# Optimization experiments

Hardware: AMD Instinct MI355X
Metric: run time of the kernel (lower is better)

Reference implementation:

```python
import jax, jax.numpy as jnp
import numpy as np

B, M, R = 2, 2048, 256
H, DH = 16, 64
ROPE_THETA = 10000.0


def setup_inputs() -> dict:
    key = jax.random.key(0)
    ks = jax.random.split(key, 9)
    d = H * DH
    inp = {
        "Pq": jax.random.normal(ks[0], (B, M, R), jnp.float32),
        "Pk": jax.random.normal(ks[1], (B, M, R), jnp.float32),
        "Pv": jax.random.normal(ks[2], (B, M, R), jnp.float32),
        "Vq": jax.random.normal(ks[3], (R, d), jnp.float32) / np.sqrt(R),
        "Vk": jax.random.normal(ks[4], (R, d), jnp.float32) / np.sqrt(R),
        "Vv": jax.random.normal(ks[5], (R, d), jnp.float32) / np.sqrt(R),
        "bq": jax.random.normal(ks[6], (d,), jnp.float32),
        "bk": jax.random.normal(ks[7], (d,), jnp.float32),
        "bv": jax.random.normal(ks[8], (d,), jnp.float32),
        "attention_mask": jnp.ones((B, M), jnp.int32),
        "position_ids": jnp.tile(jnp.arange(M, dtype=jnp.int32), (B, 1)),
    }
    return inp


def _rope_cos_sin(position_ids):
    # half-half RoPE tables; kernel only reads the first half of cos/sin
    inv_freq = 1.0 / (ROPE_THETA ** (jnp.arange(0, DH, 2, dtype=jnp.float32) / DH))
    freqs = position_ids.astype(jnp.float32)[:, :, None] * inv_freq[None, None, :]  # [B,M,DH/2]
    return jnp.cos(freqs)[:, None], jnp.sin(freqs)[:, None]  # [B,1,M,DH/2]


def _heads(P, V, b):
    # low-rank reconstruction: [B,M,R] @ [R,H*DH] + [H*DH] -> [B,H,M,DH]
    x = jnp.einsum('bmr,rd->bmd', P, V) + b
    return x.reshape(x.shape[0], x.shape[1], H, DH).transpose(0, 2, 1, 3)


def _rotate(x, cos, sin):
    x0, x1 = x[..., :DH // 2], x[..., DH // 2:]
    return jnp.concatenate([x0 * cos - x1 * sin, x0 * sin + x1 * cos], axis=-1)


def reference(Pq, Pk, Pv, Vq, Vk, Vv, bq, bk, bv, attention_mask, position_ids):
    cos, sin = _rope_cos_sin(position_ids)
    q = _rotate(_heads(Pq, Vq, bq), cos, sin)  # [B,H,M,DH]
    k = _rotate(_heads(Pk, Vk, bk), cos, sin)
    v = _heads(Pv, Vv, bv)
    scale = 1.0 / jnp.sqrt(jnp.float32(DH))
    scores = jnp.einsum('bhmd,bhnd->bhmn', q, k) * scale
    keep = attention_mask.astype(bool)[:, None, None, :]
    scores = jnp.where(keep, scores, -jnp.inf)
    # online-softmax equivalent with all-masked-row zeroing (matches kernel)
    mx = jnp.max(scores, axis=-1, keepdims=True)
    safe_mx = jnp.where(jnp.isfinite(mx), mx, 0.0)
    p = jnp.exp(scores - safe_mx)
    l = jnp.sum(p, axis=-1, keepdims=True)
    out = jnp.einsum('bhmn,bhnd->bhmd', p, v) / jnp.where(l > 0, l, 1.0)
    out = jnp.where(l > 0, out, 0.0)
    return out  # [B,H,M,DH]
```

## Files before the change

kernel.cpp:

```cpp
#include <hip/hip_runtime.h>
#include <cstdint>
#include <cstddef>

#define Bc 2
#define Mc 2048
#define Rc 256
#define Hc 16
#define DHc 64
#define Dc (Hc * DHc)
#define NKT (Mc / 64)
#define NSPLIT 2
#define NKT2 (NKT / NSPLIT)

typedef __attribute__((ext_vector_type(8))) short short8;
typedef __attribute__((ext_vector_type(4))) float float4v;
typedef __attribute__((ext_vector_type(4))) unsigned short ushort4v;
typedef __attribute__((ext_vector_type(8))) unsigned short ushort8v;
typedef __attribute__((ext_vector_type(4))) unsigned int uint4v;

#if __has_builtin(__builtin_amdgcn_exp2f)
#define EXPFN(x) __builtin_amdgcn_exp2f(x)
#define QSCALE 0.18033688f
#define MADD_KEEP (-28.8539008f)
#else
#define EXPFN(x) __expf(x)
#define QSCALE 0.125f
#define MADD_KEEP (-20.0f)
#endif

__device__ inline unsigned short f2bf(float f) {
    union { float f; uint32_t u; } v;
    v.f = f;
    uint32_t r = v.u + 0x7fffu + ((v.u >> 16) & 1u);
    return (unsigned short)(r >> 16);
}

__device__ inline int swz(int row, int chunk) {
    return row * 128 + ((chunk ^ (row & 7)) << 4);
}

__global__ __launch_bounds__(256)
void proj_kernel(const float* __restrict__ Pq, const float* __restrict__ Pk,
                 const float* __restrict__ Pv,
                 const float* __restrict__ Vq, const float* __restrict__ Vk,
                 const float* __restrict__ Vv,
                 const float* __restrict__ bq, const float* __restrict__ bk,
                 const float* __restrict__ bv,
                 const int* __restrict__ pos_ids,
                 unsigned short* __restrict__ Qb, unsigned short* __restrict__ Kb,
                 unsigned short* __restrict__ Vta)
{
    __shared__ __align__(16) unsigned char AtB[128 * 128];
    __shared__ __align__(16) unsigned char BtB[128 * 128];

    const int tid = threadIdx.x;
    const int z = blockIdx.z, mat = z >> 1, b = z & 1;
    const int m0 = blockIdx.x * 128, d0 = blockIdx.y * 128;
    const int w = tid >> 6, lane = tid & 63, col = lane & 15, quad = lane >> 4;
    const int mh = w & 1, dh2 = w >> 1;

    const float* P  = mat == 0 ? Pq : (mat == 1 ? Pk : Pv);
    const float* Vm = mat == 0 ? Vq : (mat == 1 ? Vk : Vv);
    const float* Pg = P + ((size_t)b * Mc + m0) * Rc;

    const int arow = tid >> 1, ac0 = (tid & 1) * 4;
    const int bkr = tid >> 2, bd = (tid & 3) * 32;

    float4v acc[4][4] = {};

    for (int kc = 0; kc < 4; ++kc) {
        float4 af[8], bf4[8];
        #pragma unroll
        for (int i = 0; i < 8; ++i)
            af[i] = *(const float4*)&Pg[(size_t)arow * Rc + kc * 64 + (tid & 1) * 32 + i * 4];
        #pragma unroll
        for (int i = 0; i < 8; ++i)
            bf4[i] = *(const float4*)&Vm[(size_t)(kc * 64 + bkr) * Dc + d0 + bd + i * 4];
        ushort8v ua[4];
        #pragma unroll
        for (int i = 0; i < 4; ++i) {
            float4 f0 = af[2 * i], f1 = af[2 * i + 1];
            ushort8v u = { f2bf(f0.x), f2bf(f0.y), f2bf(f0.z), f2bf(f0.w),
                           f2bf(f1.x), f2bf(f1.y), f2bf(f1.z), f2bf(f1.w) };
            ua[i] = u;
        }
        __syncthreads();
        #pragma unroll
        for (int i = 0; i < 4; ++i)
            *(ushort8v*)(AtB + swz(arow, ac0 + i)) = ua[i];
        #pragma unroll
        for (int i = 0; i < 8; ++i) {
            const float* fp = (const float*)&bf4[i];
            #pragma unroll
            for (int c = 0; c < 4; ++c) {
                int d = bd + i * 4 + c;
                *(unsigned short*)(BtB + d * 128 + (((bkr >> 3) ^ (d & 7)) << 4)
                                   + (bkr & 7) * 2) = f2bf(fp[c]);
            }
        }
        __syncthreads();

        #pragma unroll
        for (int kk = 0; kk < 2; ++kk) {
            short8 afr[4], bfr[4];
            #pragma unroll
            for (int mt = 0; mt < 4; ++mt)
                afr[mt] = *(const short8*)(AtB + swz(mh * 64 + mt * 16 + col, kk * 4 + quad));
            #pragma unroll
            for (int dt = 0; dt < 4; ++dt)
                bfr[dt] = *(const short8*)(BtB + swz(dh2 * 64 + dt * 16 + col, kk * 4 + quad));
            #pragma unroll
            for (int mt = 0; mt < 4; ++mt)
                #pragma unroll
                for (int dt = 0; dt < 4; ++dt)
                    acc[mt][dt] = __builtin_amdgcn_mfma_f32_16x16x32_bf16(
                        afr[mt], bfr[dt], acc[mt][dt], 0, 0, 0);
        }
    }

    const int head = (d0 + dh2 * 64) >> 6;
    const int bh = b * Hc + head;

    if (mat < 2) {
        const float* bias = mat == 0 ? bq : bk;
        unsigned short* outp = mat == 0 ? Qb : Kb;
        const float oscale = mat == 0 ? QSCALE : 1.0f;
        float b00 = bias[head * 64 + col],      b01 = bias[head * 64 + 16 + col];
        float b10 = bias[head * 64 + 32 + col], b11 = bias[head * 64 + 48 + col];
        float if0 = __expf(-0.28782314f * (float)col);
        float if1 = __expf(-0.28782314f * (float)(col + 16));
        #pragma unroll
        for (int mt = 0; mt < 4; ++mt)
            #pragma unroll
            for (int r = 0; r < 4; ++r) {
                int m = m0 + mh * 64 + mt * 16 + quad * 4 + r;
                float pos = (float)pos_ids[b * Mc + m];
                float a0 = pos * if0, a1 = pos * if1;
                float cs0 = __cosf(a0), sn0 = __sinf(a0);
                float cs1 = __cosf(a1), sn1 = __sinf(a1);
                float x00 = acc[mt][0][r] + b00, x10 = acc[mt][2][r] + b10;
                float x01 = acc[mt][1][r] + b01, x11 = acc[mt][3][r] + b11;
                unsigned short* og = outp + ((size_t)bh * Mc + m) * DHc;
                og[col]      = f2bf((x00 * cs0 - x10 * sn0) * oscale);
                og[32 + col] = f2bf((x00 * sn0 + x10 * cs0) * oscale);
                og[16 + col] = f2bf((x01 * cs1 - x11 * sn1) * oscale);
                og[48 + col] = f2bf((x01 * sn1 + x11 * cs1) * oscale);
            }
    } else {
        #pragma unroll
        for (int dt = 0; dt < 4; ++dt) {
            int d = d0 + dh2 * 64 + dt * 16 + col;
            float bb = bv[d];
            int dh = d & 63;
            #pragma unroll
            for (int mt = 0; mt < 4; ++mt) {
                ushort4v pv;
                #pragma unroll
                for (int r = 0; r < 4; ++r) pv[r] = f2bf(acc[mt][dt][r] + bb);
                size_t base = ((size_t)bh * DHc + dh) * Mc + m0 + mh * 64 + mt * 16 + quad * 4;
                *(ushort4v*)&Vta[base] = pv;
            }
        }
    }
}

__global__ __launch_bounds__(256, 2)
void attn_kernel(const unsigned short* __restrict__ Qb,
                 const unsigned short* __restrict__ Kb,
                 const unsigned short* __restrict__ Vt,
                 const int* __restrict__ mask,
                 float* __restrict__ O0,
                 float* __restrict__ O1,
                 float* __restrict__ lpart)
{
    __shared__ __align__(16) unsigned char KsB[64 * 128];
    __shared__ __align__(16) unsigned char VsB[64 * 128];
    __shared__ __align__(16) unsigned short Ps[4][32][72];

    const int tid = threadIdx.x;
    const int q0 = blockIdx.x * 128;
    const int bh = blockIdx.y;
    const int b  = bh >> 4;
    const int s  = blockIdx.z;
    const int w = tid >> 6, lane = tid & 63, col = lane & 15, quad = lane >> 4;

    short8 qf[2][2];
    #pragma unroll
    for (int qs = 0; qs < 2; ++qs) {
        const unsigned short* Qg =
            Qb + ((size_t)bh * Mc + q0 + w * 32 + qs * 16 + col) * DHc + quad * 8;
        qf[qs][0] = *(const short8*)Qg;
        qf[qs][1] = *(const short8*)(Qg + 32);
    }

    const int srow = tid >> 3, sc = tid & 7;
    const int dst0 = swz(srow, sc), dst1 = swz(srow + 32, sc);
    const unsigned short* Kg = Kb + (size_t)bh * Mc * DHc + (size_t)s * (Mc / 2) * DHc;
    const unsigned short* Vg = Vt + (size_t)bh * DHc * Mc + s * (Mc / 2);
    const int* mp = mask + b * Mc + s * (Mc / 2);

    uint4v kr0 = *(const uint4v*)&Kg[(size_t)srow * DHc + sc * 8];
    uint4v kr1 = *(const uint4v*)&Kg[(size_t)(srow + 32) * DHc + sc * 8];
    uint4v vr0 = *(const uint4v*)&Vg[(size_t)srow * Mc + sc * 8];
    uint4v vr1 = *(const uint4v*)&Vg[(size_t)(srow + 32) * Mc + sc * 8];

    float lsum[2] = {0.0f, 0.0f};
    float4v acc_o[2][4] = {};

    for (int kt = 0; kt < NKT2; ++kt) {
        __syncthreads();
        *(uint4v*)(KsB + dst0) = kr0; *(uint4v*)(KsB + dst1) = kr1;
        *(uint4v*)(VsB + dst0) = vr0; *(uint4v*)(VsB + dst1) = vr1;
        __syncthreads();

        if (kt + 1 < NKT2) {
            const unsigned short* Kn = Kg + (size_t)(kt + 1) * 64 * DHc;
            kr0 = *(const uint4v*)&Kn[(size_t)srow * DHc + sc * 8];
            kr1 = *(const uint4v*)&Kn[(size_t)(srow + 32) * DHc + sc * 8];
            vr0 = *(const uint4v*)&Vg[(size_t)srow * Mc + (kt + 1) * 64 + sc * 8];
            vr1 = *(const uint4v*)&Vg[(size_t)(srow + 32) * Mc + (kt + 1) * 64 + sc * 8];
        }

        int4 mv[4];
        #pragma unroll
        for (int ks = 0; ks < 4; ++ks)
            mv[ks] = *(const int4*)&mp[kt * 64 + ks * 16 + quad * 4];

        float4v sacc[4][2] = {};
        #pragma unroll
        for (int ks = 0; ks < 4; ++ks) {
            short8 a0 = *(const short8*)(KsB + swz(ks * 16 + col, quad));
            short8 a1 = *(const short8*)(KsB + swz(ks * 16 + col, 4 + quad));
            #pragma unroll
            for (int qs = 0; qs < 2; ++qs) {
                sacc[ks][qs] = __builtin_amdgcn_mfma_f32_16x16x32_bf16(
                    a0, qf[qs][0], sacc[ks][qs], 0, 0, 0);
                sacc[ks][qs] = __builtin_amdgcn_mfma_f32_16x16x32_bf16(
                    a1, qf[qs][1], sacc[ks][qs], 0, 0, 0);
            }
        }

        #pragma unroll
        for (int ks = 0; ks < 4; ++ks) {
            const int* mi = (const int*)&mv[ks];
            #pragma unroll
            for (int qs = 0; qs < 2; ++qs) {
                ushort4v pw;
                #pragma unroll
                for (int r = 0; r < 4; ++r) {
                    float madd = mi[r] ? MADD_KEEP : -1e30f;
                    float p = EXPFN(sacc[ks][qs][r] + madd);
                    lsum[qs] += p;
                    union { float f; uint32_t u; } cv; cv.f = p;
                    pw[r] = (unsigned short)((cv.u + 0x8000u) >> 16);
                }
                *(ushort4v*)&Ps[w][qs * 16 + col][ks * 16 + quad * 4] = pw;
            }
        }

        #pragma unroll
        for (int kk = 0; kk < 2; ++kk) {
            short8 pa0 = *(const short8*)&Ps[w][col][kk * 32 + quad * 8];
            short8 pa1 = *(const short8*)&Ps[w][16 + col][kk * 32 + quad * 8];
            #pragma unroll
            for (int ds = 0; ds < 4; ++ds) {
                short8 vb = *(const short8*)(VsB + swz(ds * 16 + col, kk * 4 + quad));
                acc_o[0][ds] = __builtin_amdgcn_mfma_f32_16x16x32_bf16(
                    pa0, vb, acc_o[0][ds], 0, 0, 0);
                acc_o[1][ds] = __builtin_amdgcn_mfma_f32_16x16x32_bf16(
                    pa1, vb, acc_o[1][ds], 0, 0, 0);
            }
        }
    }

    #pragma unroll
    for (int qs = 0; qs < 2; ++qs) {
        lsum[qs] += __shfl_xor(lsum[qs], 16);
        lsum[qs] += __shfl_xor(lsum[qs], 32);
    }

    float* Opart = (s == 0) ? O0 : O1;
    #pragma unroll
    for (int qs = 0; qs < 2; ++qs)
        #pragma unroll
        for (int r = 0; r < 4; ++r) {
            int m = q0 + w * 32 + qs * 16 + quad * 4 + r;
            float* og = Opart + ((size_t)bh * Mc + m) * DHc;
            #pragma unroll
            for (int ds = 0; ds < 4; ++ds)
                og[ds * 16 + col] = acc_o[qs][ds][r];
        }
    if (quad == 0) {
        #pragma unroll
        for (int qs = 0; qs < 2; ++qs)
            lpart[((size_t)s * Bc * Hc + bh) * Mc + q0 + w * 32 + qs * 16 + col] = lsum[qs];
    }
}

__global__ __launch_bounds__(256)
void combine_kernel(float* __restrict__ out, const float* __restrict__ O1,
                    const float* __restrict__ lpart)
{
    size_t i = ((size_t)blockIdx.x * 256 + threadIdx.x) * 4;
    int row = (int)(i >> 6);
    float sl = lpart[row] + lpart[(size_t)Bc * Hc * Mc + row];
    float inv = (sl > 0.0f) ? 1.0f / sl : 0.0f;
    float4 a = *(const float4*)&out[i];
    const float4 bb = *(const float4*)&O1[i];
    a.x = (a.x + bb.x) * inv;
    a.y = (a.y + bb.y) * inv;
    a.z = (a.z + bb.z) * inv;
    a.w = (a.w + bb.w) * inv;
    *(float4*)&out[i] = a;
}

extern "C" void kernel_launch(void* const* d_in, const int* in_sizes, int n_in,
                              void* d_out, int out_size, void* d_ws, size_t ws_size,
                              hipStream_t stream) {
    const float* Pq = (const float*)d_in[0];
    const float* Pk = (const float*)d_in[1];
    const float* Pv = (const float*)d_in[2];
    const float* Vq = (const float*)d_in[3];
    const float* Vk = (const float*)d_in[4];
    const float* Vv = (const float*)d_in[5];
    const float* bq = (const float*)d_in[6];
    const float* bk = (const float*)d_in[7];
    const float* bv = (const float*)d_in[8];
    const int*   am = (const int*)d_in[9];
    const int*   pid = (const int*)d_in[10];
    float* out = (float*)d_out;

    const size_t n_el = (size_t)Bc * Hc * Mc * DHc;
    unsigned short* Qb  = (unsigned short*)d_ws;
    unsigned short* Kb  = Qb + n_el;
    unsigned short* Vta = Kb + n_el;
    float* O1    = (float*)(Vta + n_el);
    float* lpart = O1 + n_el;

    dim3 blk(256);
    proj_kernel<<<dim3(Mc / 128, Dc / 128, 6), blk, 0, stream>>>(
        Pq, Pk, Pv, Vq, Vk, Vv, bq, bk, bv, pid, Qb, Kb, Vta);

    attn_kernel<<<dim3(Mc / 128, Bc * Hc, NSPLIT), blk, 0, stream>>>(
        Qb, Kb, Vta, am, out, O1, lpart);

    combine_kernel<<<dim3((unsigned)(n_el / 1024)), blk, 0, stream>>>(out, O1, lpart);
}
```

Before: 180.2 us.

## Split KV inside attention block, fuse combine, pre-transpose V weights to bf16

The attention kernel no longer uses a grid-level KV split with a separate combine kernel. Each block now has two wave pairs, each pair handling half of the keys, and the partial outputs and row sums are merged through shared memory before the normalized result is written. A new transpose_v kernel converts the V projection weights to bf16 in transposed layout once, so the projection kernel loads them with vector copies instead of scalar scattered converting stores. This removes a launch and the fp32 partial-output round trip through global memory. In exchange the attention grid is half as large, and each block uses 64KB of shared memory plus more accumulator registers, which may lower occupancy.

```diff
diff --git a/kernel.cpp b/kernel.cpp
--- a/kernel.cpp
+++ b/kernel.cpp
@@ -8,9 +8,7 @@
 #define Hc 16
 #define DHc 64
 #define Dc (Hc * DHc)
-#define NKT (Mc / 64)
-#define NSPLIT 2
-#define NKT2 (NKT / NSPLIT)
+#define NKT2 16
 
 typedef __attribute__((ext_vector_type(8))) short short8;
 typedef __attribute__((ext_vector_type(4))) float float4v;
@@ -40,10 +38,24 @@
 }
 
 __global__ __launch_bounds__(256)
+void transpose_v(const float* __restrict__ V0, const float* __restrict__ V1,
+                 const float* __restrict__ V2, unsigned short* __restrict__ Vt)
+{
+    const int mat = blockIdx.z;
+    const float* src = mat == 0 ? V0 : (mat == 1 ? V1 : V2);
+    const int d  = blockIdx.x * 256 + threadIdx.x;
+    const int kg = blockIdx.y;
+    short8 v;
+    #pragma unroll
+    for (int j = 0; j < 8; ++j)
+        v[j] = (short)f2bf(src[(size_t)(kg * 8 + j) * Dc + d]);
+    *(short8*)&Vt[((size_t)mat * Dc + d) * Rc + kg * 8] = v;
+}
+
+__global__ __launch_bounds__(256)
 void proj_kernel(const float* __restrict__ Pq, const float* __restrict__ Pk,
                  const float* __restrict__ Pv,
-                 const float* __restrict__ Vq, const float* __restrict__ Vk,
-                 const float* __restrict__ Vv,
+                 const unsigned short* __restrict__ Vtp,
                  const float* __restrict__ bq, const float* __restrict__ bk,
                  const float* __restrict__ bv,
                  const int* __restrict__ pos_ids,
@@ -59,23 +71,24 @@
     const int w = tid >> 6, lane = tid & 63, col = lane & 15, quad = lane >> 4;
     const int mh = w & 1, dh2 = w >> 1;
 
-    const float* P  = mat == 0 ? Pq : (mat == 1 ? Pk : Pv);
-    const float* Vm = mat == 0 ? Vq : (mat == 1 ? Vk : Vv);
+    const float* P = mat == 0 ? Pq : (mat == 1 ? Pk : Pv);
     const float* Pg = P + ((size_t)b * Mc + m0) * Rc;
+    const unsigned short* Vg = Vtp + (size_t)mat * Dc * Rc + (size_t)d0 * Rc;
 
     const int arow = tid >> 1, ac0 = (tid & 1) * 4;
-    const int bkr = tid >> 2, bd = (tid & 3) * 32;
+    const int brow = tid >> 1, bc0 = (tid & 1) * 4;
 
     float4v acc[4][4] = {};
 
     for (int kc = 0; kc < 4; ++kc) {
-        float4 af[8], bf4[8];
+        float4 af[8];
+        uint4v br[4];
         #pragma unroll
         for (int i = 0; i < 8; ++i)
             af[i] = *(const float4*)&Pg[(size_t)arow * Rc + kc * 64 + (tid & 1) * 32 + i * 4];
         #pragma unroll
-        for (int i = 0; i < 8; ++i)
-            bf4[i] = *(const float4*)&Vm[(size_t)(kc * 64 + bkr) * Dc + d0 + bd + i * 4];
+        for (int i = 0; i < 4; ++i)
+            br[i] = *(const uint4v*)&Vg[(size_t)brow * Rc + kc * 64 + (bc0 + i) * 8];
         ushort8v ua[4];
         #pragma unroll
         for (int i = 0; i < 4; ++i) {
@@ -86,17 +99,9 @@
         }
         __syncthreads();
         #pragma unroll
-        for (int i = 0; i < 4; ++i)
+        for (int i = 0; i < 4; ++i) {
             *(ushort8v*)(AtB + swz(arow, ac0 + i)) = ua[i];
-        #pragma unroll
-        for (int i = 0; i < 8; ++i) {
-            const float* fp = (const float*)&bf4[i];
-            #pragma unroll
-            for (int c = 0; c < 4; ++c) {
-                int d = bd + i * 4 + c;
-                *(unsigned short*)(BtB + d * 128 + (((bkr >> 3) ^ (d & 7)) << 4)
-                                   + (bkr & 7) * 2) = f2bf(fp[c]);
-            }
+            *(uint4v*)(BtB + swz(brow, bc0 + i)) = br[i];
         }
         __syncthreads();
 
@@ -169,149 +174,151 @@
                  const unsigned short* __restrict__ Kb,
                  const unsigned short* __restrict__ Vt,
                  const int* __restrict__ mask,
-                 float* __restrict__ O0,
-                 float* __restrict__ O1,
-                 float* __restrict__ lpart)
+                 float* __restrict__ out)
 {
-    __shared__ __align__(16) unsigned char KsB[64 * 128];
-    __shared__ __align__(16) unsigned char VsB[64 * 128];
-    __shared__ __align__(16) unsigned short Ps[4][32][72];
+    __shared__ __align__(16) unsigned char smem[65536];
 
     const int tid = threadIdx.x;
     const int q0 = blockIdx.x * 128;
     const int bh = blockIdx.y;
     const int b  = bh >> 4;
-    const int s  = blockIdx.z;
     const int w = tid >> 6, lane = tid & 63, col = lane & 15, quad = lane >> 4;
-
-    short8 qf[2][2];
+    const int s = w >> 1, qh = w & 1;
+
+    unsigned char* KsB = smem + s * 8192;
+    unsigned char* VsB = smem + 16384 + s * 8192;
+    unsigned char* PsB = smem + 32768 + w * 8192;
+
+    short8 qf[4][2];
     #pragma unroll
-    for (int qs = 0; qs < 2; ++qs) {
+    for (int qg = 0; qg < 4; ++qg) {
         const unsigned short* Qg =
-            Qb + ((size_t)bh * Mc + q0 + w * 32 + qs * 16 + col) * DHc + quad * 8;
-        qf[qs][0] = *(const short8*)Qg;
-        qf[qs][1] = *(const short8*)(Qg + 32);
-    }
-
-    const int srow = tid >> 3, sc = tid & 7;
-    const int dst0 = swz(srow, sc), dst1 = swz(srow + 32, sc);
-    const unsigned short* Kg = Kb + (size_t)bh * Mc * DHc + (size_t)s * (Mc / 2) * DHc;
+            Qb + ((size_t)bh * Mc + q0 + qh * 64 + qg * 16 + col) * DHc + quad * 8;
+        qf[qg][0] = *(const short8*)Qg;
+        qf[qg][1] = *(const short8*)(Qg + 32);
+    }
+
+    const int ts = tid & 127;
+    const int srow = ts >> 1, sc0 = (ts & 1) * 4;
+    const unsigned short* Kg = Kb + ((size_t)bh * Mc + s * (Mc / 2)) * DHc;
     const unsigned short* Vg = Vt + (size_t)bh * DHc * Mc + s * (Mc / 2);
     const int* mp = mask + b * Mc + s * (Mc / 2);
 
-    uint4v kr0 = *(const uint4v*)&Kg[(size_t)srow * DHc + sc * 8];
-    uint4v kr1 = *(const uint4v*)&Kg[(size_t)(srow + 32) * DHc + sc * 8];
-    uint4v vr0 = *(const uint4v*)&Vg[(size_t)srow * Mc + sc * 8];
-    uint4v vr1 = *(const uint4v*)&Vg[(size_t)(srow + 32) * Mc + sc * 8];
-
-    float lsum[2] = {0.0f, 0.0f};
-    float4v acc_o[2][4] = {};
+    uint4v kr[4], vr[4];
+    #pragma unroll
+    for (int i = 0; i < 4; ++i) {
+        kr[i] = *(const uint4v*)&Kg[(size_t)srow * DHc + (sc0 + i) * 8];
+        vr[i] = *(const uint4v*)&Vg[(size_t)srow * Mc + (sc0 + i) * 8];
+    }
+
+    float lsum[4] = {};
+    float4v acc_o[4][4] = {};
 
     for (int kt = 0; kt < NKT2; ++kt) {
         __syncthreads();
-        *(uint4v*)(KsB + dst0) = kr0; *(uint4v*)(KsB + dst1) = kr1;
-        *(uint4v*)(VsB + dst0) = vr0; *(uint4v*)(VsB + dst1) = vr1;
+        #pragma unroll
+        for (int i = 0; i < 4; ++i) {
+            *(uint4v*)(KsB + swz(srow, sc0 + i)) = kr[i];
+            *(uint4v*)(VsB + swz(srow, sc0 + i)) = vr[i];
+        }
         __syncthreads();
 
         if (kt + 1 < NKT2) {
             const unsigned short* Kn = Kg + (size_t)(kt + 1) * 64 * DHc;
-            kr0 = *(const uint4v*)&Kn[(size_t)srow * DHc + sc * 8];
-            kr1 = *(const uint4v*)&Kn[(size_t)(srow + 32) * DHc + sc * 8];
-            vr0 = *(const uint4v*)&Vg[(size_t)srow * Mc + (kt + 1) * 64 + sc * 8];
-            vr1 = *(const uint4v*)&Vg[(size_t)(srow + 32) * Mc + (kt + 1) * 64 + sc * 8];
-        }
-
-        int4 mv[4];
-        #pragma unroll
-        for (int ks = 0; ks < 4; ++ks)
-            mv[ks] = *(const int4*)&mp[kt * 64 + ks * 16 + quad * 4];
-
-        float4v sacc[4][2] = {};
+            #pragma unroll
+            for (int i = 0; i < 4; ++i) {
+                kr[i] = *(const uint4v*)&Kn[(size_t)srow * DHc + (sc0 + i) * 8];
+                vr[i] = *(const uint4v*)&Vg[(size_t)srow * Mc + (kt + 1) * 64 + (sc0 + i) * 8];
+            }
+        }
+
         #pragma unroll
         for (int ks = 0; ks < 4; ++ks) {
+            int4 mv = *(const int4*)&mp[kt * 64 + ks * 16 + quad * 4];
+            const int* mi = (const int*)&mv;
+            float md[4];
+            #pragma unroll
+            for (int r = 0; r < 4; ++r) md[r] = mi[r] ? MADD_KEEP : -1e30f;
             short8 a0 = *(const short8*)(KsB + swz(ks * 16 + col, quad));
             short8 a1 = *(const short8*)(KsB + swz(ks * 16 + col, 4 + quad));
             #pragma unroll
-            for (int qs = 0; qs < 2; ++qs) {
-                sacc[ks][qs] = __builtin_amdgcn_mfma_f32_16x16x32_bf16(
-                    a0, qf[qs][0], sacc[ks][qs], 0, 0, 0);
-                sacc[ks][qs] = __builtin_amdgcn_mfma_f32_16x16x32_bf16(
-                    a1, qf[qs][1], sacc[ks][qs], 0, 0, 0);
-            }
-        }
-
-        #pragma unroll
-        for (int ks = 0; ks < 4; ++ks) {
-            const int* mi = (const int*)&mv[ks];
-            #pragma unroll
-            for (int qs = 0; qs < 2; ++qs) {
+            for (int qg = 0; qg < 4; ++qg) {
+                float4v sacc = {};
+                sacc = __builtin_amdgcn_mfma_f32_16x16x32_bf16(a0, qf[qg][0], sacc, 0, 0, 0);
+                sacc = __builtin_amdgcn_mfma_f32_16x16x32_bf16(a1, qf[qg][1], sacc, 0, 0, 0);
                 ushort4v pw;
                 #pragma unroll
                 for (int r = 0; r < 4; ++r) {
-                    float madd = mi[r] ? MADD_KEEP : -1e30f;
-                    float p = EXPFN(sacc[ks][qs][r] + madd);
-                    lsum[qs] += p;
+                    float p = EXPFN(sacc[r] + md[r]);
+                    lsum[qg] += p;
                     union { float f; uint32_t u; } cv; cv.f = p;
                     pw[r] = (unsigned short)((cv.u + 0x8000u) >> 16);
                 }
-                *(ushort4v*)&Ps[w][qs * 16 + col][ks * 16 + quad * 4] = pw;
+                int qrow = qg * 16 + col;
+                *(ushort4v*)(PsB + qrow * 128 +
+                             (((ks * 2 + (quad >> 1)) ^ (qrow & 7)) << 4) +
+                             (quad & 1) * 8) = pw;
             }
         }
 
         #pragma unroll
         for (int kk = 0; kk < 2; ++kk) {
-            short8 pa0 = *(const short8*)&Ps[w][col][kk * 32 + quad * 8];
-            short8 pa1 = *(const short8*)&Ps[w][16 + col][kk * 32 + quad * 8];
-            #pragma unroll
-            for (int ds = 0; ds < 4; ++ds) {
-                short8 vb = *(const short8*)(VsB + swz(ds * 16 + col, kk * 4 + quad));
-                acc_o[0][ds] = __builtin_amdgcn_mfma_f32_16x16x32_bf16(
-                    pa0, vb, acc_o[0][ds], 0, 0, 0);
-                acc_o[1][ds] = __builtin_amdgcn_mfma_f32_16x16x32_bf16(
-                    pa1, vb, acc_o[1][ds], 0, 0, 0);
+            short8 pa[4];
+            #pragma unroll
+            for (int qg = 0; qg < 4; ++qg)
+                pa[qg] = *(const short8*)(PsB + swz(qg * 16 + col, kk * 4 + quad));
+            #pragma unroll
+            for (int dh = 0; dh < 4; ++dh) {
+                short8 vb = *(const short8*)(VsB + swz(dh * 16 + col, kk * 4 + quad));
+                #pragma unroll
+                for (int qg = 0; qg < 4; ++qg)
+                    acc_o[qg][dh] = __builtin_amdgcn_mfma_f32_16x16x32_bf16(
+                        pa[qg], vb, acc_o[qg][dh], 0, 0, 0);
             }
         }
     }
 
     #pragma unroll
-    for (int qs = 0; qs < 2; ++qs) {
-        lsum[qs] += __shfl_xor(lsum[qs], 16);
-        lsum[qs] += __shfl_xor(lsum[qs], 32);
-    }
-
-    float* Opart = (s == 0) ? O0 : O1;
-    #pragma unroll
-    for (int qs = 0; qs < 2; ++qs)
-        #pragma unroll
-        for (int r = 0; r < 4; ++r) {
-            int m = q0 + w * 32 + qs * 16 + quad * 4 + r;
-            float* og = Opart + ((size_t)bh * Mc + m) * DHc;
-            #pragma unroll
-            for (int ds = 0; ds < 4; ++ds)
-                og[ds * 16 + col] = acc_o[qs][ds][r];
-        }
-    if (quad == 0) {
-        #pragma unroll
-        for (int qs = 0; qs < 2; ++qs)
-            lpart[((size_t)s * Bc * Hc + bh) * Mc + q0 + w * 32 + qs * 16 + col] = lsum[qs];
-    }
-}
-
-__global__ __launch_bounds__(256)
-void combine_kernel(float* __restrict__ out, const float* __restrict__ O1,
-                    const float* __restrict__ lpart)
-{
-    size_t i = ((size_t)blockIdx.x * 256 + threadIdx.x) * 4;
-    int row = (int)(i >> 6);
-    float sl = lpart[row] + lpart[(size_t)Bc * Hc * Mc + row];
-    float inv = (sl > 0.0f) ? 1.0f / sl : 0.0f;
-    float4 a = *(const float4*)&out[i];
-    const float4 bb = *(const float4*)&O1[i];
-    a.x = (a.x + bb.x) * inv;
-    a.y = (a.y + bb.y) * inv;
-    a.z = (a.z + bb.z) * inv;
-    a.w = (a.w + bb.w) * inv;
-    *(float4*)&out[i] = a;
+    for (int qg = 0; qg < 4; ++qg) {
+        lsum[qg] += __shfl_xor(lsum[qg], 16);
+        lsum[qg] += __shfl_xor(lsum[qg], 32);
+    }
+
+    __syncthreads();
+    float* Of = (float*)(smem + 32768 + qh * 16384);
+    float* Lf = (float*)smem;
+    if (s == 1) {
+        #pragma unroll
+        for (int qg = 0; qg < 4; ++qg)
+            #pragma unroll
+            for (int dh = 0; dh < 4; ++dh)
+                #pragma unroll
+                for (int r = 0; r < 4; ++r)
+                    Of[(qg * 16 + quad * 4 + r) * 64 + dh * 16 + col] = acc_o[qg][dh][r];
+        if (quad == 0) {
+            #pragma unroll
+            for (int qg = 0; qg < 4; ++qg)
+                Lf[qh * 64 + qg * 16 + col] = lsum[qg];
+        }
+    }
+    __syncthreads();
+    if (s == 0) {
+        #pragma unroll
+        for (int qg = 0; qg < 4; ++qg)
+            #pragma unroll
+            for (int r = 0; r < 4; ++r) {
+                float l0 = __shfl(lsum[qg], quad * 4 + r);
+                float l1 = Lf[qh * 64 + qg * 16 + quad * 4 + r];
+                float lt = l0 + l1;
+                float inv = (lt > 0.0f) ? 1.0f / lt : 0.0f;
+                int m = q0 + qh * 64 + qg * 16 + quad * 4 + r;
+                float* og = out + ((size_t)bh * Mc + m) * DHc;
+                #pragma unroll
+                for (int dh = 0; dh < 4; ++dh)
+                    og[dh * 16 + col] =
+                        (acc_o[qg][dh][r] + Of[(qg * 16 + quad * 4 + r) * 64 + dh * 16 + col]) * inv;
+            }
+    }
 }
 
 extern "C" void kernel_launch(void* const* d_in, const int* in_sizes, int n_in,
@@ -334,15 +341,13 @@
     unsigned short* Qb  = (unsigned short*)d_ws;
     unsigned short* Kb  = Qb + n_el;
     unsigned short* Vta = Kb + n_el;
-    float* O1    = (float*)(Vta + n_el);
-    float* lpart = O1 + n_el;
+    unsigned short* Vtp = Vta + n_el;
 
     dim3 blk(256);
+    transpose_v<<<dim3(Dc / 256, Rc / 8, 3), blk, 0, stream>>>(Vq, Vk, Vv, Vtp);
+
     proj_kernel<<<dim3(Mc / 128, Dc / 128, 6), blk, 0, stream>>>(
-        Pq, Pk, Pv, Vq, Vk, Vv, bq, bk, bv, pid, Qb, Kb, Vta);
-
-    attn_kernel<<<dim3(Mc / 128, Bc * Hc, NSPLIT), blk, 0, stream>>>(
-        Qb, Kb, Vta, am, out, O1, lpart);
-
-    combine_kernel<<<dim3((unsigned)(n_el / 1024)), blk, 0, stream>>>(out, O1, lpart);
-}
+        Pq, Pk, Pv, Vtp, bq, bk, bv, pid, Qb, Kb, Vta);
+
+    attn_kernel<<<dim3(Mc / 128, Bc * Hc), blk, 0, stream>>>(Qb, Kb, Vta, am, out);
+}
```

Measured after the change: 175.5 us. -2.6%, faster.
